# Performance work log

Measured on AMD Instinct MI355X. Metric: run time of the kernel, lower is better.

## Reference

```python
import jax, jax.numpy as jnp
import numpy as np

B, H, N, M, S, R, BANKS = 64, 1024, 65536, 64, 3, 4, 4
EPS_COS = 1e-8   # cosine-similarity epsilon
EPS_NORM = 1e-5  # final weight normalization epsilon (from original code)


def setup_inputs() -> dict:
    key = jax.random.key(0)
    ks = jax.random.split(key, 12)
    w = lambda k, s: jax.random.normal(k, s, jnp.float32) * 0.02
    return dict(
        h_t=jax.random.normal(ks[0], (B, H), jnp.float32),
        ww=jax.nn.softmax(jax.random.uniform(ks[1], (B, N), jnp.float32), axis=-1),
        wr=jax.nn.softmax(jax.random.uniform(ks[2], (R, B, N), jnp.float32), axis=-1),
        memory=jax.random.uniform(ks[3], (BANKS, N, M), jnp.float32) * 0.1,
        key_w=w(ks[4], (H, M)), key_b=jnp.zeros((M,), jnp.float32),
        beta_w=w(ks[5], (H, 1)), beta_b=jnp.zeros((1,), jnp.float32),
        gate_w=w(ks[6], (H, 1)), gate_b=jnp.zeros((1,), jnp.float32),
        shift_w=w(ks[7], (H, S)), shift_b=jnp.zeros((S,), jnp.float32),
        gamma_w=w(ks[8], (H, 1)), gamma_b=jnp.zeros((1,), jnp.float32),
        erase_w=w(ks[9], (H, M)), erase_b=jnp.zeros((M,), jnp.float32),
        add_w=w(ks[10], (H, M)), add_b=jnp.zeros((M,), jnp.float32),
        bank_no=0,
    )


def _weight_update(h, w_tm1, m, key_w, key_b, beta_w, beta_b, gate_w, gate_b,
                   shift_w, shift_b, gamma_w, gamma_b):
    # h: [B,H], w_tm1: [B,N], m: [N,M]
    k = jnp.clip(h @ key_w + key_b, 0.0, 1.0)            # [B,M] key
    beta = jax.nn.relu(h @ beta_w + beta_b)              # [B,1] sharpness
    g = jnp.clip(h @ gate_w + gate_b, 0.0, 1.0)          # [B,1] interpolation gate
    s = jax.nn.softmax(h @ shift_w + shift_b, axis=-1)   # [B,S] shift kernel
    gamma = 1.0 + jax.nn.relu(h @ gamma_w + gamma_b)     # [B,1] sharpening power
    # content addressing: cosine similarity of key against each memory row
    kn = k / (jnp.linalg.norm(k, axis=1, keepdims=True) + EPS_COS)
    mn = m / (jnp.linalg.norm(m, axis=1, keepdims=True) + EPS_COS)
    sim = kn @ mn.T                                      # [B,N]
    w_c = jax.nn.softmax(sim * beta, axis=-1)            # [B,N]
    w_g = g * w_c + (1.0 - g) * w_tm1                    # gated interpolation
    # per-sample 1D shift (cross-correlation, zero-padded to keep length N)
    pad_l = S // 2
    w_pad = jnp.pad(w_g, ((0, 0), (pad_l, S - 1 - pad_l)))
    shifted = jnp.stack([w_pad[:, j:j + N] for j in range(S)], axis=1)  # [B,S,N]
    w_tilde = jnp.einsum('bs,bsn->bn', s, shifted)
    # power sharpening; normalization by GLOBAL sum (quirk of the original code)
    w_pow = w_tilde ** gamma
    return w_pow / (jnp.sum(w_pow) + EPS_NORM)


def reference(h_t, ww, wr, memory, key_w, key_b, beta_w, beta_b, gate_w, gate_b,
              shift_w, shift_b, gamma_w, gamma_b, erase_w, erase_b, add_w, add_b,
              bank_no):
    m0 = memory[bank_no]                                  # [N,M]
    wu = lambda w_prev, m: _weight_update(
        h_t, w_prev, m, key_w, key_b, beta_w, beta_b, gate_w, gate_b,
        shift_w, shift_b, gamma_w, gamma_b)
    # write head
    ww_new = wu(ww, m0)                                   # [B,N]
    e = jnp.clip(h_t @ erase_w + erase_b, 0.0, 1.0)       # [B,M] erase vec
    a = jnp.clip(jax.nn.relu(h_t @ add_w + add_b), 0.0, 1.0)  # [B,M] add vec
    # batched outer-product erase/add (replaces the python torch.ger loop)
    mem_erase = jnp.einsum('bn,bm->nm', ww_new, e)
    mem_add = jnp.einsum('bn,bm->nm', ww_new, a)
    m1 = m0 * (1.0 - mem_erase) + mem_add                 # [N,M]
    # read heads (vmapped over num_reads)
    wr_new = jax.vmap(lambda wp: wu(wp, m1))(wr)          # [R,B,N]
    r = jnp.einsum('rbn,nm->rbm', wr_new, m1)             # [R,B,M]
    r_t = jnp.transpose(r, (1, 0, 2)).reshape(B, R * M)   # cat along dim 1
    return r_t
```

## Files before the change

kernel.cpp:

```cpp
#include <hip/hip_runtime.h>

#define NN 65536
#define BB 64
#define HH 1024
#define MM 64
#define RR 4

__device__ __forceinline__ float waveReduceSum(float v) {
#pragma unroll
  for (int off = 32; off > 0; off >>= 1) v += __shfl_xor(v, off, 64);
  return v;
}

__device__ __forceinline__ float fastPow(float wt, float p) {
  return __expf(p * __logf(wt));
}

__global__ __launch_bounds__(256) void prep1_kernel(
    const float* __restrict__ h_t,
    const float* __restrict__ key_w, const float* __restrict__ erase_w,
    const float* __restrict__ add_w,
    float* __restrict__ prep_part,
    float* __restrict__ RS0p, float* __restrict__ RS1p, float* __restrict__ GSp)
{
  const int b = blockIdx.y;
  const int mat = blockIdx.x >> 2, chunk = blockIdx.x & 3;
  const int t = threadIdx.x;
  if (mat == 0 && chunk == 0) { RS0p[b * 256 + t] = 0.f; RS1p[b * 256 + t] = 0.f; }
  if (mat == 0 && chunk == 1 && b < 20) GSp[b * 256 + t] = 0.f;

  const float* Wm = (mat == 0) ? key_w : ((mat == 1) ? erase_w : add_w);
  const int c = t & 63, q = t >> 6;
  const int h0 = chunk * 256 + q * 64;
  float d = 0.f;
#pragma unroll 8
  for (int i = 0; i < 64; i++)
    d += h_t[b * HH + h0 + i] * Wm[(h0 + i) * 64 + c];
  __shared__ float red[64][5];
  red[c][q] = d;
  __syncthreads();
  if (t < 64)
    prep_part[((b * 3 + mat) * 4 + chunk) * 64 + t] =
        red[t][0] + red[t][1] + red[t][2] + red[t][3];
}

__global__ __launch_bounds__(256) void prep2_kernel(
    const float* __restrict__ h_t, const float* __restrict__ prep_part,
    const float* __restrict__ key_b,
    const float* __restrict__ beta_w, const float* __restrict__ beta_b,
    const float* __restrict__ gate_w, const float* __restrict__ gate_b,
    const float* __restrict__ shift_w, const float* __restrict__ shift_b,
    const float* __restrict__ gamma_w, const float* __restrict__ gamma_b,
    const float* __restrict__ erase_b, const float* __restrict__ add_b,
    float* __restrict__ kn, float* __restrict__ e_v, float* __restrict__ a_v,
    float* __restrict__ g, float* __restrict__ gamma_,
    float* __restrict__ s, float* __restrict__ betaGlob)
{
  const int b = blockIdx.x;
  const int t = threadIdx.x;
  __shared__ float k_sh[64];
  if (t < 192) {
    const int mat = t >> 6, c = t & 63;
    const float* pp = prep_part + ((b * 3 + mat) * 4) * 64 + c;
    const float v = pp[0] + pp[64] + pp[128] + pp[192];
    if (mat == 0) k_sh[c] = fminf(fmaxf(v + key_b[c], 0.f), 1.f);
    else if (mat == 1) e_v[b * 64 + c] = fminf(fmaxf(v + erase_b[c], 0.f), 1.f);
    else a_v[b * 64 + c] = fminf(fmaxf(v + add_b[c], 0.f), 1.f);
  } else {
    const int lane = t - 192;
    float o0 = 0.f, o1 = 0.f, o2 = 0.f, o3 = 0.f, o4 = 0.f, o5 = 0.f;
#pragma unroll 4
    for (int k = 0; k < 16; k++) {
      const int hh = lane + k * 64;
      const float hv = h_t[b * HH + hh];
      o0 += hv * beta_w[hh];
      o1 += hv * gate_w[hh];
      o2 += hv * gamma_w[hh];
      o3 += hv * shift_w[hh * 3 + 0];
      o4 += hv * shift_w[hh * 3 + 1];
      o5 += hv * shift_w[hh * 3 + 2];
    }
    o0 = waveReduceSum(o0); o1 = waveReduceSum(o1); o2 = waveReduceSum(o2);
    o3 = waveReduceSum(o3); o4 = waveReduceSum(o4); o5 = waveReduceSum(o5);
    if (lane == 0) {
      betaGlob[b] = fmaxf(o0 + beta_b[0], 0.f);
      g[b]        = fminf(fmaxf(o1 + gate_b[0], 0.f), 1.f);
      gamma_[b]   = 1.0f + fmaxf(o2 + gamma_b[0], 0.f);
      const float l0 = o3 + shift_b[0], l1 = o4 + shift_b[1], l2 = o5 + shift_b[2];
      const float mx = fmaxf(l0, fmaxf(l1, l2));
      const float e0 = __expf(l0 - mx), e1 = __expf(l1 - mx), e2 = __expf(l2 - mx);
      const float inv = 1.f / (e0 + e1 + e2);
      s[b * 3 + 0] = e0 * inv; s[b * 3 + 1] = e1 * inv; s[b * 3 + 2] = e2 * inv;
    }
  }
  __syncthreads();
  if (t < 64) {
    float ss = 0.f;
    for (int j = 0; j < 64; j++) ss += k_sh[j] * k_sh[j];
    kn[b * 64 + t] = k_sh[t] / (sqrtf(ss) + 1e-8f);
  }
}

__global__ __launch_bounds__(256, 4) void content_kernel(
    const float* __restrict__ mem, const int* __restrict__ bank,
    const float* __restrict__ kn, const float* __restrict__ beta,
    float* __restrict__ E, float* __restrict__ RSp)
{
  const float* Mrow = mem + (bank ? ((size_t)(*bank) * (size_t)NN * MM) : (size_t)0);
  const int t = threadIdx.x;
  const int lane = t & 63;
  const int n = blockIdx.x * 64 + lane;
  const int bq = t >> 6;

  float4 row[16];
  const float4* rp = (const float4*)(Mrow + (size_t)n * MM);
#pragma unroll
  for (int q = 0; q < 16; q++) row[q] = rp[q];
  float s0 = 0.f, s1 = 0.f, s2 = 0.f, s3 = 0.f;
#pragma unroll
  for (int q = 0; q < 16; q++) {
    s0 += row[q].x * row[q].x; s1 += row[q].y * row[q].y;
    s2 += row[q].z * row[q].z; s3 += row[q].w * row[q].w;
  }
  const float rinv = 1.0f / (sqrtf((s0 + s1) + (s2 + s3)) + 1e-8f);

#pragma unroll 2
  for (int i = 0; i < 16; i++) {
    const int rb = __builtin_amdgcn_readfirstlane(bq * 16 + i);
    const float4* kp = (const float4*)(kn + rb * 64);
    float d0 = 0.f, d1 = 0.f, d2 = 0.f, d3 = 0.f;
#pragma unroll
    for (int q = 0; q < 16; q++) {
      const float4 kq = kp[q];
      d0 += kq.x * row[q].x; d1 += kq.y * row[q].y;
      d2 += kq.z * row[q].z; d3 += kq.w * row[q].w;
    }
    const float e = __expf(beta[rb] * ((d0 + d1) + (d2 + d3)) * rinv);
    E[(size_t)rb * NN + n] = e;
    const float r = waveReduceSum(e);
    if (lane == 0)
      atomicAdd(&RSp[rb * 256 + (blockIdx.x & 15) * 16], r);
  }
}

template <int NR>
__global__ __launch_bounds__(256) void wpow_all_kernel(
    const float* __restrict__ E, const float* __restrict__ wprev,
    const float* __restrict__ RSp, const float* __restrict__ g,
    const float* __restrict__ gamma_, const float* __restrict__ s,
    float* __restrict__ Wout, float* __restrict__ GSp, int slot0)
{
  const int b = blockIdx.y;
  const float gb = g[b], gmb = gamma_[b];
  const float s0 = s[b * 3], s1 = s[b * 3 + 1], s2 = s[b * 3 + 2];
  float rs = 0.f;
#pragma unroll
  for (int j = 0; j < 16; j++) rs += RSp[b * 256 + j * 16];
  const float grinv = gb / rs;
  const float omg = 1.f - gb;

  const int t = threadIdx.x, lane = t & 63, w = t >> 6;
  const int n4 = blockIdx.x * 1024 + 4 * t;

  const float* Eb = E + (size_t)b * NN;
  const float4 ev = *((const float4*)(Eb + n4));
  const float gex = grinv * ev.x, gey = grinv * ev.y;
  const float gez = grinv * ev.z, gew = grinv * ev.w;
  float geL = 0.f, geR = 0.f;
  if (lane == 0 && n4 > 0) geL = grinv * Eb[n4 - 1];
  if (lane == 63 && n4 + 4 < NN) geR = grinv * Eb[n4 + 4];

  float gs_local[NR];
#pragma unroll
  for (int j = 0; j < NR; j++) gs_local[j] = 0.f;

#pragma unroll
  for (int j = 0; j < NR; j++) {
    const float* wb = wprev + ((size_t)j * BB + b) * NN;
    const float4 wv = *((const float4*)(wb + n4));
    float4 wgc;
    wgc.x = gex + omg * wv.x;
    wgc.y = gey + omg * wv.y;
    wgc.z = gez + omg * wv.z;
    wgc.w = gew + omg * wv.w;
    float up = __shfl_up(wgc.w, 1, 64);
    float dn = __shfl_down(wgc.x, 1, 64);
    if (lane == 0)  up = (n4 > 0)       ? (geL + omg * wb[n4 - 1]) : 0.f;
    if (lane == 63) dn = (n4 + 4 < NN)  ? (geR + omg * wb[n4 + 4]) : 0.f;
    float4 wt;
    wt.x = s0 * up    + s1 * wgc.x + s2 * wgc.y;
    wt.y = s0 * wgc.x + s1 * wgc.y + s2 * wgc.z;
    wt.z = s0 * wgc.y + s1 * wgc.z + s2 * wgc.w;
    wt.w = s0 * wgc.z + s1 * wgc.w + s2 * dn;
    float4 wp;
    wp.x = fastPow(wt.x, gmb); wp.y = fastPow(wt.y, gmb);
    wp.z = fastPow(wt.z, gmb); wp.w = fastPow(wt.w, gmb);
    *((float4*)(Wout + ((size_t)j * BB + b) * NN + n4)) = wp;
    gs_local[j] += wp.x + wp.y + wp.z + wp.w;
  }

  __shared__ float wsum[4][NR];
#pragma unroll
  for (int j = 0; j < NR; j++) {
    const float v = waveReduceSum(gs_local[j]);
    if (lane == 0) wsum[w][j] = v;
  }
  __syncthreads();
  if (t < NR)
    atomicAdd(&GSp[(slot0 + t) * 1024 + b * 16],
              wsum[0][t] + wsum[1][t] + wsum[2][t] + wsum[3][t]);
}

__global__ __launch_bounds__(256) void apply_write_kernel(
    const float* __restrict__ W0, const float* __restrict__ GSp,
    const float* __restrict__ e_v, const float* __restrict__ a_v,
    const float* __restrict__ memory, const int* __restrict__ bank,
    float* __restrict__ m1)
{
  __shared__ float cw[64 * 68];
  __shared__ float e_sh[4096];
  __shared__ float a_sh[4096];
  const int t = threadIdx.x;
  const int n0 = blockIdx.x * 64;
  float gs = 0.f;
#pragma unroll
  for (int j = 0; j < 64; j++) gs += GSp[j * 16];
  const float invGS = 1.0f / (gs + 1e-5f);
#pragma unroll
  for (int q = 0; q < 4; q++) {
    ((float4*)e_sh)[t + 256 * q] = ((const float4*)e_v)[t + 256 * q];
    ((float4*)a_sh)[t + 256 * q] = ((const float4*)a_v)[t + 256 * q];
  }
#pragma unroll
  for (int rep = 0; rep < 4; rep++) {
    const int idx = rep * 256 + t;
    const int b = idx >> 4, nc = idx & 15;
    float4 v = *((const float4*)(W0 + (size_t)b * NN + n0 + nc * 4));
    v.x *= invGS; v.y *= invGS; v.z *= invGS; v.w *= invGS;
    *((float4*)&cw[b * 68 + nc * 4]) = v;
  }
  __syncthreads();
  const int nl = t >> 2, mq = t & 3;
  const int n = n0 + nl;
  float er[16], ad[16];
#pragma unroll
  for (int j = 0; j < 16; j++) { er[j] = 0.f; ad[j] = 0.f; }
  for (int b = 0; b < 64; b++) {
    const float c = cw[b * 68 + nl];
#pragma unroll
    for (int j = 0; j < 4; j++) {
      const float4 ev = *((const float4*)&e_sh[b * 64 + mq * 16 + j * 4]);
      const float4 av = *((const float4*)&a_sh[b * 64 + mq * 16 + j * 4]);
      er[j * 4 + 0] += c * ev.x; er[j * 4 + 1] += c * ev.y;
      er[j * 4 + 2] += c * ev.z; er[j * 4 + 3] += c * ev.w;
      ad[j * 4 + 0] += c * av.x; ad[j * 4 + 1] += c * av.y;
      ad[j * 4 + 2] += c * av.z; ad[j * 4 + 3] += c * av.w;
    }
  }
  const float* M0 = memory + (size_t)(*bank) * (size_t)NN * MM;
  const float4* m0p = (const float4*)(M0 + (size_t)n * MM + mq * 16);
  float4* m1p = (float4*)(m1 + (size_t)n * MM + mq * 16);
#pragma unroll
  for (int j = 0; j < 4; j++) {
    const float4 mv = m0p[j];
    float4 o;
    o.x = mv.x * (1.f - er[j * 4 + 0]) + ad[j * 4 + 0];
    o.y = mv.y * (1.f - er[j * 4 + 1]) + ad[j * 4 + 1];
    o.z = mv.z * (1.f - er[j * 4 + 2]) + ad[j * 4 + 2];
    o.w = mv.w * (1.f - er[j * 4 + 3]) + ad[j * 4 + 3];
    m1p[j] = o;
  }
}

__global__ __launch_bounds__(256, 2) void wpow_gemm_kernel(
    const float* __restrict__ E, const float* __restrict__ wr,
    const float* __restrict__ RSp, const float* __restrict__ g,
    const float* __restrict__ gamma_, const float* __restrict__ s,
    const float* __restrict__ m1, float* __restrict__ part,
    float* __restrict__ GSp)
{
  __shared__ float m1_sh[64][68];
  __shared__ float ge_sh[64][68];
  __shared__ float w0_sh[64][68];
  __shared__ float w1_sh[64][68];
  __shared__ float geL[64], geR[64];
  __shared__ float wv0L[64], wv0R[64], wv1L[64], wv1R[64];
  __shared__ float rinv_sh[64], omg_sh[64], gm_sh[64];
  __shared__ float s0_sh[64], s1_sh[64], s2_sh[64];
  __shared__ float wsum[4][2];

  const int t = threadIdx.x;
  const int w = t >> 6, lane = t & 63;
  const int mq = t & 15, bq = t >> 4;
  const int n0 = blockIdx.x * 128;
  const int r0 = blockIdx.y * 2;
  const float* wr0 = wr + (size_t)r0 * BB * NN;
  const float* wr1 = wr + (size_t)(r0 + 1) * BB * NN;

  if (t < 64) {
    float rs = 0.f;
#pragma unroll
    for (int j = 0; j < 16; j++) rs += RSp[t * 256 + j * 16];
    const float gb = g[t];
    rinv_sh[t] = gb / rs;
    omg_sh[t]  = 1.f - gb;
    gm_sh[t]   = gamma_[t];
    s0_sh[t] = s[t * 3 + 0];
    s1_sh[t] = s[t * 3 + 1];
    s2_sh[t] = s[t * 3 + 2];
  }

  float4 acc[2][4];
#pragma unroll
  for (int rr = 0; rr < 2; rr++)
#pragma unroll
    for (int j = 0; j < 4; j++) acc[rr][j] = make_float4(0.f, 0.f, 0.f, 0.f);
  float gs_acc[2] = {0.f, 0.f};

  for (int sub = 0; sub < 2; ++sub) {
    const int nb = n0 + sub * 64;
    __syncthreads();

#pragma unroll
    for (int rep = 0; rep < 4; rep++) {
      const int row = rep * 16 + bq;
      *((float4*)&m1_sh[row][mq * 4]) =
          ((const float4*)(m1 + (size_t)(nb + row) * MM))[mq];
      const float gr = rinv_sh[row];
      const float4 e4 = *((const float4*)(E + (size_t)row * NN + nb + mq * 4));
      float4 ge4;
      ge4.x = gr * e4.x; ge4.y = gr * e4.y; ge4.z = gr * e4.z; ge4.w = gr * e4.w;
      *((float4*)&ge_sh[row][mq * 4]) = ge4;
      *((float4*)&w0_sh[row][mq * 4]) =
          *((const float4*)(wr0 + (size_t)row * NN + nb + mq * 4));
      *((float4*)&w1_sh[row][mq * 4]) =
          *((const float4*)(wr1 + (size_t)row * NN + nb + mq * 4));
    }
    if (t < 64) {
      geL[t] = (nb > 0) ? rinv_sh[t] * E[(size_t)t * NN + nb - 1] : 0.f;
    } else if (t < 128) {
      const int b = t - 64;
      geR[b] = (nb + 64 < NN) ? rinv_sh[b] * E[(size_t)b * NN + nb + 64] : 0.f;
    } else if (t < 192) {
      const int b = t - 128;
      wv0L[b] = (nb > 0) ? wr0[(size_t)b * NN + nb - 1] : 0.f;
      wv1L[b] = (nb > 0) ? wr1[(size_t)b * NN + nb - 1] : 0.f;
    } else {
      const int b = t - 192;
      wv0R[b] = (nb + 64 < NN) ? wr0[(size_t)b * NN + nb + 64] : 0.f;
      wv1R[b] = (nb + 64 < NN) ? wr1[(size_t)b * NN + nb + 64] : 0.f;
    }
    __syncthreads();

    float4 wp0[4], wp1[4];
    float ls0 = 0.f, ls1 = 0.f;
#pragma unroll
    for (int rep = 0; rep < 4; rep++) {
      const int b = rep * 16 + bq;
      const int n4 = mq * 4;
      const float omg = omg_sh[b];
      const float c0 = s0_sh[b], c1 = s1_sh[b], c2 = s2_sh[b];
      const float gm = gm_sh[b];
      const float4 ge4 = *((const float4*)&ge_sh[b][n4]);
      {
        const float4 wv4 = *((const float4*)&w0_sh[b][n4]);
        const float wg0 = ge4.x + omg * wv4.x;
        const float wg1 = ge4.y + omg * wv4.y;
        const float wg2 = ge4.z + omg * wv4.z;
        const float wg3 = ge4.w + omg * wv4.w;
        const float wgm = (n4 == 0)
            ? (geL[b] + omg * wv0L[b])
            : (ge_sh[b][n4 - 1] + omg * w0_sh[b][n4 - 1]);
        const float wgp = (n4 == 60)
            ? (geR[b] + omg * wv0R[b])
            : (ge_sh[b][n4 + 4] + omg * w0_sh[b][n4 + 4]);
        wp0[rep].x = fastPow(c0 * wgm + c1 * wg0 + c2 * wg1, gm);
        wp0[rep].y = fastPow(c0 * wg0 + c1 * wg1 + c2 * wg2, gm);
        wp0[rep].z = fastPow(c0 * wg1 + c1 * wg2 + c2 * wg3, gm);
        wp0[rep].w = fastPow(c0 * wg2 + c1 * wg3 + c2 * wgp, gm);
        ls0 += (wp0[rep].x + wp0[rep].y) + (wp0[rep].z + wp0[rep].w);
      }
      {
        const float4 wv4 = *((const float4*)&w1_sh[b][n4]);
        const float wg0 = ge4.x + omg * wv4.x;
        const float wg1 = ge4.y + omg * wv4.y;
        const float wg2 = ge4.z + omg * wv4.z;
        const float wg3 = ge4.w + omg * wv4.w;
        const float wgm = (n4 == 0)
            ? (geL[b] + omg * wv1L[b])
            : (ge_sh[b][n4 - 1] + omg * w1_sh[b][n4 - 1]);
        const float wgp = (n4 == 60)
            ? (geR[b] + omg * wv1R[b])
            : (ge_sh[b][n4 + 4] + omg * w1_sh[b][n4 + 4]);
        wp1[rep].x = fastPow(c0 * wgm + c1 * wg0 + c2 * wg1, gm);
        wp1[rep].y = fastPow(c0 * wg0 + c1 * wg1 + c2 * wg2, gm);
        wp1[rep].z = fastPow(c0 * wg1 + c1 * wg2 + c2 * wg3, gm);
        wp1[rep].w = fastPow(c0 * wg2 + c1 * wg3 + c2 * wgp, gm);
        ls1 += (wp1[rep].x + wp1[rep].y) + (wp1[rep].z + wp1[rep].w);
      }
    }
    gs_acc[0] += ls0;
    gs_acc[1] += ls1;
    __syncthreads();

#pragma unroll
    for (int rep = 0; rep < 4; rep++) {
      const int row = rep * 16 + bq;
      *((float4*)&w0_sh[row][mq * 4]) = wp0[rep];
      *((float4*)&w1_sh[row][mq * 4]) = wp1[rep];
    }
    __syncthreads();

#pragma unroll 2
    for (int c4 = 0; c4 < 16; c4++) {
      const int nn = c4 * 4;
      const float4 mv0 = *((const float4*)&m1_sh[nn + 0][mq * 4]);
      const float4 mv1 = *((const float4*)&m1_sh[nn + 1][mq * 4]);
      const float4 mv2 = *((const float4*)&m1_sh[nn + 2][mq * 4]);
      const float4 mv3 = *((const float4*)&m1_sh[nn + 3][mq * 4]);
#pragma unroll
      for (int j = 0; j < 4; j++) {
        const float4 w0j = *((const float4*)&w0_sh[bq * 4 + j][nn]);
        float4& a0 = acc[0][j];
        a0.x += w0j.x * mv0.x + w0j.y * mv1.x + w0j.z * mv2.x + w0j.w * mv3.x;
        a0.y += w0j.x * mv0.y + w0j.y * mv1.y + w0j.z * mv2.y + w0j.w * mv3.y;
        a0.z += w0j.x * mv0.z + w0j.y * mv1.z + w0j.z * mv2.z + w0j.w * mv3.z;
        a0.w += w0j.x * mv0.w + w0j.y * mv1.w + w0j.z * mv2.w + w0j.w * mv3.w;
        const float4 w1j = *((const float4*)&w1_sh[bq * 4 + j][nn]);
        float4& a1 = acc[1][j];
        a1.x += w1j.x * mv0.x + w1j.y * mv1.x + w1j.z * mv2.x + w1j.w * mv3.x;
        a1.y += w1j.x * mv0.y + w1j.y * mv1.y + w1j.z * mv2.y + w1j.w * mv3.y;
        a1.z += w1j.x * mv0.z + w1j.y * mv1.z + w1j.z * mv2.z + w1j.w * mv3.z;
        a1.w += w1j.x * mv0.w + w1j.y * mv1.w + w1j.z * mv2.w + w1j.w * mv3.w;
      }
    }
  }
#pragma unroll
  for (int rr = 0; rr < 2; rr++)
#pragma unroll
    for (int j = 0; j < 4; j++)
      *((float4*)&part[((size_t)blockIdx.x * 4 + r0 + rr) * 4096 +
                       (bq * 4 + j) * 64 + mq * 4]) = acc[rr][j];
#pragma unroll
  for (int rr = 0; rr < 2; rr++) {
    const float v = waveReduceSum(gs_acc[rr]);
    if (lane == 0) wsum[w][rr] = v;
  }
  __syncthreads();
  if (t < 2)
    atomicAdd(&GSp[(1 + r0 + t) * 1024],
              wsum[0][t] + wsum[1][t] + wsum[2][t] + wsum[3][t]);
}

__global__ __launch_bounds__(1024) void reduce_norm_kernel(
    const float* __restrict__ part, const float* __restrict__ GSp,
    float* __restrict__ out)
{
  const int t = threadIdx.x;
  const int ln = t & 63, wv = t >> 6;
  const int off = blockIdx.x * 64 + ln;
  const int r = blockIdx.x >> 6;
  float sm = 0.f;
#pragma unroll 8
  for (int k = wv; k < 512; k += 16) sm += part[(size_t)k * 16384 + off];
  __shared__ float red[16][64];
  red[wv][ln] = sm;
  __syncthreads();
  if (t < 64) {
    const float gv = GSp[(1 + r) * 1024];
    float sum = 0.f;
#pragma unroll
    for (int j = 0; j < 16; j++) sum += red[j][t];
    const int off2 = blockIdx.x * 64 + t;
    const int b = (off2 >> 6) & 63, m = off2 & 63;
    out[b * 256 + r * 64 + m] = sum / (gv + 1e-5f);
  }
}

extern "C" void kernel_launch(void* const* d_in, const int* in_sizes, int n_in,
                              void* d_out, int out_size, void* d_ws, size_t ws_size,
                              hipStream_t stream) {
  (void)in_sizes; (void)n_in; (void)out_size; (void)ws_size;
  const float* h_t    = (const float*)d_in[0];
  const float* ww     = (const float*)d_in[1];
  const float* wr     = (const float*)d_in[2];
  const float* memory = (const float*)d_in[3];
  const float* key_w  = (const float*)d_in[4];
  const float* key_b  = (const float*)d_in[5];
  const float* beta_w = (const float*)d_in[6];
  const float* beta_b = (const float*)d_in[7];
  const float* gate_w = (const float*)d_in[8];
  const float* gate_b = (const float*)d_in[9];
  const float* shift_w = (const float*)d_in[10];
  const float* shift_b = (const float*)d_in[11];
  const float* gamma_w = (const float*)d_in[12];
  const float* gamma_b = (const float*)d_in[13];
  const float* erase_w = (const float*)d_in[14];
  const float* erase_b = (const float*)d_in[15];
  const float* add_w   = (const float*)d_in[16];
  const float* add_b   = (const float*)d_in[17];
  const int*   bank    = (const int*)d_in[18];

  float* ws = (float*)d_ws;
  float* E0    = ws;
  float* part  = ws;
  float* W0    = ws + 4194304;
  float* m1    = ws + 8388608;
  float* E1    = ws + 12582912;
  float* smallb  = ws + 16777216;
  float* kn       = smallb + 16384;
  float* e_v      = smallb + 20480;
  float* a_v      = smallb + 24576;
  float* betaB    = smallb + 28672;
  float* g        = smallb + 28736;
  float* gam      = smallb + 28800;
  float* s        = smallb + 28864;
  float* RS0p     = smallb + 29120;
  float* RS1p     = smallb + 45504;
  float* GSp      = smallb + 61888;
  float* prep_part = smallb + 67008;

  prep1_kernel<<<dim3(12, 64), 256, 0, stream>>>(h_t, key_w, erase_w, add_w,
                                                 prep_part, RS0p, RS1p, GSp);
  prep2_kernel<<<64, 256, 0, stream>>>(h_t, prep_part, key_b,
                                       beta_w, beta_b, gate_w, gate_b,
                                       shift_w, shift_b, gamma_w, gamma_b,
                                       erase_b, add_b,
                                       kn, e_v, a_v, g, gam, s, betaB);
  content_kernel<<<1024, 256, 0, stream>>>(memory, bank, kn, betaB, E0, RS0p);
  wpow_all_kernel<1><<<dim3(64, 64), 256, 0, stream>>>(E0, ww, RS0p, g, gam, s,
                                                       W0, GSp, 0);
  apply_write_kernel<<<1024, 256, 0, stream>>>(W0, GSp, e_v, a_v, memory, bank, m1);
  content_kernel<<<1024, 256, 0, stream>>>(m1, nullptr, kn, betaB, E1, RS1p);
  wpow_gemm_kernel<<<dim3(512, 2), 256, 0, stream>>>(E1, wr, RS1p, g, gam, s,
                                                     m1, part, GSp);
  reduce_norm_kernel<<<256, 1024, 0, stream>>>(part, GSp, (float*)d_out);
}
```

Measured before the change: 176.8 us.

## Register-prefetch next tile in wpow_gemm and halve its grid

The read-head wpow_gemm kernel now handles 256 N-columns per block (four 64-wide sub-tiles) instead of 128, and loads the next sub-tile's m1, E, wr0 and wr1 data plus the halo values into registers while the current sub-tile is computed. The goal is to hide global-load latency behind compute and to halve the number of partial sums that reduce_norm has to combine. The cost is higher register pressure, which may reduce occupancy, and only 512 blocks in the grid, which gives less parallelism across the GPU.

```diff
diff --git a/kernel.cpp b/kernel.cpp
--- a/kernel.cpp
+++ b/kernel.cpp
@@ -292,7 +292,7 @@
   const int t = threadIdx.x;
   const int w = t >> 6, lane = t & 63;
   const int mq = t & 15, bq = t >> 4;
-  const int n0 = blockIdx.x * 128;
+  const int n0 = blockIdx.x * 256;
   const int r0 = blockIdx.y * 2;
   const float* wr0 = wr + (size_t)r0 * BB * NN;
   const float* wr1 = wr + (size_t)(r0 + 1) * BB * NN;
@@ -317,40 +317,64 @@
     for (int j = 0; j < 4; j++) acc[rr][j] = make_float4(0.f, 0.f, 0.f, 0.f);
   float gs_acc[2] = {0.f, 0.f};
 
-  for (int sub = 0; sub < 2; ++sub) {
+  float4 pf_m1[4], pf_e[4], pf_w0[4], pf_w1[4];
+  float pf_h0 = 0.f, pf_h1 = 0.f;
+
+  auto prefetch = [&](int nb) {
+#pragma unroll
+    for (int rep = 0; rep < 4; rep++) {
+      const int row = rep * 16 + bq;
+      pf_m1[rep] = ((const float4*)(m1 + (size_t)(nb + row) * MM))[mq];
+      pf_e[rep]  = *((const float4*)(E + (size_t)row * NN + nb + mq * 4));
+      pf_w0[rep] = *((const float4*)(wr0 + (size_t)row * NN + nb + mq * 4));
+      pf_w1[rep] = *((const float4*)(wr1 + (size_t)row * NN + nb + mq * 4));
+    }
+    if (t < 64) {
+      pf_h0 = (nb > 0) ? E[(size_t)t * NN + nb - 1] : 0.f;
+    } else if (t < 128) {
+      const int b = t - 64;
+      pf_h0 = (nb + 64 < NN) ? E[(size_t)b * NN + nb + 64] : 0.f;
+    } else if (t < 192) {
+      const int b = t - 128;
+      pf_h0 = (nb > 0) ? wr0[(size_t)b * NN + nb - 1] : 0.f;
+      pf_h1 = (nb > 0) ? wr1[(size_t)b * NN + nb - 1] : 0.f;
+    } else {
+      const int b = t - 192;
+      pf_h0 = (nb + 64 < NN) ? wr0[(size_t)b * NN + nb + 64] : 0.f;
+      pf_h1 = (nb + 64 < NN) ? wr1[(size_t)b * NN + nb + 64] : 0.f;
+    }
+  };
+
+  prefetch(n0);
+
+  for (int sub = 0; sub < 4; ++sub) {
     const int nb = n0 + sub * 64;
     __syncthreads();
 
 #pragma unroll
     for (int rep = 0; rep < 4; rep++) {
       const int row = rep * 16 + bq;
-      *((float4*)&m1_sh[row][mq * 4]) =
-          ((const float4*)(m1 + (size_t)(nb + row) * MM))[mq];
+      *((float4*)&m1_sh[row][mq * 4]) = pf_m1[rep];
       const float gr = rinv_sh[row];
-      const float4 e4 = *((const float4*)(E + (size_t)row * NN + nb + mq * 4));
       float4 ge4;
-      ge4.x = gr * e4.x; ge4.y = gr * e4.y; ge4.z = gr * e4.z; ge4.w = gr * e4.w;
+      ge4.x = gr * pf_e[rep].x; ge4.y = gr * pf_e[rep].y;
+      ge4.z = gr * pf_e[rep].z; ge4.w = gr * pf_e[rep].w;
       *((float4*)&ge_sh[row][mq * 4]) = ge4;
-      *((float4*)&w0_sh[row][mq * 4]) =
-          *((const float4*)(wr0 + (size_t)row * NN + nb + mq * 4));
-      *((float4*)&w1_sh[row][mq * 4]) =
-          *((const float4*)(wr1 + (size_t)row * NN + nb + mq * 4));
+      *((float4*)&w0_sh[row][mq * 4]) = pf_w0[rep];
+      *((float4*)&w1_sh[row][mq * 4]) = pf_w1[rep];
     }
     if (t < 64) {
-      geL[t] = (nb > 0) ? rinv_sh[t] * E[(size_t)t * NN + nb - 1] : 0.f;
+      geL[t] = rinv_sh[t] * pf_h0;
     } else if (t < 128) {
-      const int b = t - 64;
-      geR[b] = (nb + 64 < NN) ? rinv_sh[b] * E[(size_t)b * NN + nb + 64] : 0.f;
+      geR[t - 64] = rinv_sh[t - 64] * pf_h0;
     } else if (t < 192) {
-      const int b = t - 128;
-      wv0L[b] = (nb > 0) ? wr0[(size_t)b * NN + nb - 1] : 0.f;
-      wv1L[b] = (nb > 0) ? wr1[(size_t)b * NN + nb - 1] : 0.f;
+      wv0L[t - 128] = pf_h0; wv1L[t - 128] = pf_h1;
     } else {
-      const int b = t - 192;
-      wv0R[b] = (nb + 64 < NN) ? wr0[(size_t)b * NN + nb + 64] : 0.f;
-      wv1R[b] = (nb + 64 < NN) ? wr1[(size_t)b * NN + nb + 64] : 0.f;
+      wv0R[t - 192] = pf_h0; wv1R[t - 192] = pf_h1;
     }
     __syncthreads();
+
+    if (sub < 3) prefetch(nb + 64);
 
     float4 wp0[4], wp1[4];
     float ls0 = 0.f, ls1 = 0.f;
@@ -462,7 +486,7 @@
   const int r = blockIdx.x >> 6;
   float sm = 0.f;
 #pragma unroll 8
-  for (int k = wv; k < 512; k += 16) sm += part[(size_t)k * 16384 + off];
+  for (int k = wv; k < 256; k += 16) sm += part[(size_t)k * 16384 + off];
   __shared__ float red[16][64];
   red[wv][ln] = sm;
   __syncthreads();
@@ -532,7 +556,7 @@
                                                        W0, GSp, 0);
   apply_write_kernel<<<1024, 256, 0, stream>>>(W0, GSp, e_v, a_v, memory, bank, m1);
   content_kernel<<<1024, 256, 0, stream>>>(m1, nullptr, kn, betaB, E1, RS1p);
-  wpow_gemm_kernel<<<dim3(512, 2), 256, 0, stream>>>(E1, wr, RS1p, g, gam, s,
+  wpow_gemm_kernel<<<dim3(256, 2), 256, 0, stream>>>(E1, wr, RS1p, g, gam, s,
                                                      m1, part, GSp);
   reduce_norm_kernel<<<256, 1024, 0, stream>>>(part, GSp, (float*)d_out);
 }
```

After: 194.3 us. 1.1x slower.
